# Optimization experiments

Measured on AMD Instinct MI355X. Metric: run time of the kernel, lower is better.

Reference implementation:

```python
import jax, jax.numpy as jnp
import numpy as np

C1 = C2 = COUT = 32
LMAX = 2
N = 8192
FEAT1 = 2 * (1 + 3 + 9) * C1  # 832
WBLK = COUT * C1 * C2


def _enumerate_paths(Lmax):
    paths = []
    for L1 in range(Lmax + 1):
        for L2 in range(Lmax + 1):
            for k in range(min(L1, L2) + 1):
                Lout = L1 + L2 - 2 * k
                if 0 <= Lout <= Lmax:
                    paths.append((L1, L2, Lout, k, False))
            if L1 >= 1 and L2 >= 1:
                for k in range(min(L1 - 1, L2 - 1) + 1):
                    Lout = L1 + L2 - 2 * k - 1
                    if 0 <= Lout <= Lmax:
                        paths.append((L1, L2, Lout, k, True))
    return paths


def _path_eq(L1, L2, k, use_eps):
    # Canonical einsum for one path, fused with the weight mixing 'Zab'
    letters = 'abcdefghijklmnopqrstuvwxyz'
    tl = [c for c in letters if c not in ('a', 'b')]
    i_idx = tl[:L1]
    j_idx = tl[L1:L1 + L2]
    pos = L1 + L2
    for r in range(k):  # pairwise delta contractions on trailing indices
        j_idx[L2 - k + r] = i_idx[L1 - k + r]
    i_free = i_idx[:L1 - k]
    j_free = j_idx[:L2 - k]
    eps_terms = []
    if use_eps:
        ie, je = i_free[-1], j_free[-1]
        i_free, j_free = i_free[:-1], j_free[:-1]
        p = tl[pos]
        eps_terms = [p + ie + je]
        out_idx = i_free + j_free + [p]
    else:
        out_idx = i_free + j_free
    in_terms = ['...a' + ''.join(i_idx), '...b' + ''.join(j_idx)] + eps_terms + ['Zab']
    eq = ','.join(in_terms) + '->...Z' + ''.join(out_idx)
    return eq, len(out_idx)


def _epsilon(dtype):
    e = np.zeros((3, 3, 3), np.float32)
    e[0, 1, 2] = e[1, 2, 0] = e[2, 0, 1] = 1.0
    e[0, 2, 1] = e[2, 1, 0] = e[1, 0, 2] = -1.0
    return jnp.asarray(e, dtype=dtype)


def _split(x, C, Lmax):
    # blocks keyed (s, L): s=0 true tensor, s=1 pseudotensor
    batch = x.shape[:-1]
    out = {}
    idx = 0
    for s in (0, 1):
        for L in range(Lmax + 1):
            d = C * 3 ** L
            blk = x[..., idx:idx + d]
            idx += d
            out[(s, L)] = blk.reshape(*batch, C, *((3,) * L))
    return out


def _forward(x1, x2, weight):
    batch = x1.shape[:-1]
    A = _split(x1, C1, LMAX)
    B = _split(x2, C2, LMAX)
    eps = _epsilon(x1.dtype)
    out = {(s, L): jnp.zeros(batch + (COUT,) + (3,) * L, x1.dtype)
           for s in (0, 1) for L in range(LMAX + 1)}
    w_idx = 0
    for (L1, L2, Lout, k, ue) in _enumerate_paths(LMAX):
        eq, _ = _path_eq(L1, L2, k, ue)
        for s1 in (0, 1):
            for s2 in (0, 1):
                Wp = weight[w_idx:w_idx + WBLK].reshape(COUT, C1, C2)
                w_idx += WBLK
                t1 = A[(s1, L1)]
                t2 = B[(s2, L2)]
                if ue:
                    out_c = jnp.einsum(eq, t1, t2, eps, Wp)
                else:
                    out_c = jnp.einsum(eq, t1, t2, Wp)
                s_out = s1 ^ s2 ^ (1 if ue else 0)
                out[(s_out, Lout)] = out[(s_out, Lout)] + out_c
    parts = [out[(s, L)].reshape(*batch, COUT * 3 ** L)
             for s in (0, 1) for L in range(LMAX + 1)]
    return jnp.concatenate(parts, axis=-1)


def setup_inputs() -> dict:
    key = jax.random.key(0)
    k1, k2, k3 = jax.random.split(key, 3)
    n_paths = len(_enumerate_paths(LMAX))  # 15
    wn = n_paths * 4 * WBLK  # 1966080
    x1 = jax.random.normal(k1, (N, FEAT1), dtype=jnp.float32)
    x2 = jax.random.normal(k2, (N, FEAT1), dtype=jnp.float32)
    weight = jax.random.normal(k3, (wn,), dtype=jnp.float32) * 0.02
    return {"x1": x1, "x2": x2, "weight": weight}


def reference(x1, x2, weight):
    return _forward(x1, x2, weight)
```

## Files before the change

### kernel.cpp

```cpp
#include <hip/hip_runtime.h>

#define DEVINL __device__ __forceinline__

typedef unsigned int  uint32;
typedef unsigned short u16;

typedef short bf16x8  __attribute__((ext_vector_type(8)));
typedef float f32x16  __attribute__((ext_vector_type(16)));
typedef float fx2     __attribute__((ext_vector_type(2)));

union U4H { uint4 u; bf16x8 h; };

constexpr int PL1c[15] = {0,0,0,1,1,1,1,1,1,2,2,2,2,2,2};
constexpr int PL2c[15] = {0,1,2,0,1,1,1,2,2,0,1,1,2,2,2};
constexpr int PLOc[15] = {0,1,2,1,2,0,1,1,2,2,1,2,2,0,1};
constexpr int PTc [15] = {1,1,1,1,1,3,2,3,2,1,3,2,3,9,6};
constexpr int PW3c[3]  = {1,3,9};
constexpr int LOFFc[3] = {0,32,128};

constexpr int GCNT[6] = {6,6,12,12,12,12};
constexpr int GNT [6] = {1,1,3,3,9,9};
__device__ const int g_combo[6][12][3] = {
  {{0,0,0},{0,1,1},{5,0,0},{5,1,1},{13,0,0},{13,1,1},
   {0,0,0},{0,0,0},{0,0,0},{0,0,0},{0,0,0},{0,0,0}},
  {{0,0,1},{0,1,0},{5,0,1},{5,1,0},{13,0,1},{13,1,0},
   {0,0,0},{0,0,0},{0,0,0},{0,0,0},{0,0,0},{0,0,0}},
  {{1,0,0},{1,1,1},{3,0,0},{3,1,1},{7,0,0},{7,1,1},{10,0,0},{10,1,1},
   {6,0,1},{6,1,0},{14,0,1},{14,1,0}},
  {{1,0,1},{1,1,0},{3,0,1},{3,1,0},{7,0,1},{7,1,0},{10,0,1},{10,1,0},
   {6,0,0},{6,1,1},{14,0,0},{14,1,1}},
  {{2,0,0},{2,1,1},{4,0,0},{4,1,1},{9,0,0},{9,1,1},{12,0,0},{12,1,1},
   {8,0,1},{8,1,0},{11,0,1},{11,1,0}},
  {{2,0,1},{2,1,0},{4,0,1},{4,1,0},{9,0,1},{9,1,0},{12,0,1},{12,1,0},
   {8,0,0},{8,1,1},{11,0,0},{11,1,1}},
};

struct Terms { int iA[9]; int jB[9]; int sg[9]; };

DEVINL Terms make_terms(int path, int mo) {
  Terms t{};
  switch (path) {
    case 0:  t.iA[0]=0;  t.jB[0]=0;  t.sg[0]=1; break;
    case 1:  t.iA[0]=0;  t.jB[0]=mo; t.sg[0]=1; break;
    case 2:  t.iA[0]=0;  t.jB[0]=mo; t.sg[0]=1; break;
    case 3:  t.iA[0]=mo; t.jB[0]=0;  t.sg[0]=1; break;
    case 4:  t.iA[0]=mo/3; t.jB[0]=mo%3; t.sg[0]=1; break;
    case 5:  for (int v=0;v<3;++v){t.iA[v]=v; t.jB[v]=v; t.sg[v]=1;} break;
    case 6:  {int p=mo,u1=(p+1)%3,u2=(p+2)%3;
              t.iA[0]=u1; t.jB[0]=u2; t.sg[0]= 1;
              t.iA[1]=u2; t.jB[1]=u1; t.sg[1]=-1;} break;
    case 7:  {int x=mo; for(int u=0;u<3;++u){t.iA[u]=u; t.jB[u]=3*x+u; t.sg[u]=1;}} break;
    case 8:  {int x=mo/3,p=mo%3,u1=(p+1)%3,u2=(p+2)%3;
              t.iA[0]=u1; t.jB[0]=3*x+u2; t.sg[0]= 1;
              t.iA[1]=u2; t.jB[1]=3*x+u1; t.sg[1]=-1;} break;
    case 9:  t.iA[0]=mo; t.jB[0]=0; t.sg[0]=1; break;
    case 10: {int u=mo; for(int v=0;v<3;++v){t.iA[v]=3*u+v; t.jB[v]=v; t.sg[v]=1;}} break;
    case 11: {int u=mo/3,p=mo%3,v1=(p+1)%3,v2=(p+2)%3;
              t.iA[0]=3*u+v1; t.jB[0]=v2; t.sg[0]= 1;
              t.iA[1]=3*u+v2; t.jB[1]=v1; t.sg[1]=-1;} break;
    case 12: {int u=mo/3,x=mo%3; for(int v=0;v<3;++v){t.iA[v]=3*u+v; t.jB[v]=3*x+v; t.sg[v]=1;}} break;
    case 13: for (int w=0;w<9;++w){t.iA[w]=w; t.jB[w]=w; t.sg[w]=1;} break;
    case 14: {int p=mo,u1=(p+1)%3,u2=(p+2)%3;
              for(int v=0;v<3;++v){
                t.iA[2*v]  =3*u1+v; t.jB[2*v]  =3*u2+v; t.sg[2*v]  = 1;
                t.iA[2*v+1]=3*u2+v; t.jB[2*v+1]=3*u1+v; t.sg[2*v+1]=-1;}} break;
  }
  return t;
}

DEVINL u16 f2bf(float f) {
  uint32 u = __float_as_uint(f);
  u += 0x7fffu + ((u >> 16) & 1u);
  return (u16)(u >> 16);
}
DEVINL float bf2f(u16 h) { return __uint_as_float(((uint32)h) << 16); }

DEVINL void unpack8(uint4 r, fx2 out[4]) {
  uint32 c[4] = {r.x, r.y, r.z, r.w};
#pragma unroll
  for (int q = 0; q < 4; ++q) {
    out[q].x = __uint_as_float(c[q] << 16);
    out[q].y = __uint_as_float(c[q] & 0xffff0000u);
  }
}

DEVINL bf16x8 packA(const fx2 p[4]) {
  U4H r;
  r.u.x = __builtin_amdgcn_perm(__float_as_uint(p[0].y), __float_as_uint(p[0].x), 0x07060302u);
  r.u.y = __builtin_amdgcn_perm(__float_as_uint(p[1].y), __float_as_uint(p[1].x), 0x07060302u);
  r.u.z = __builtin_amdgcn_perm(__float_as_uint(p[2].y), __float_as_uint(p[2].x), 0x07060302u);
  r.u.w = __builtin_amdgcn_perm(__float_as_uint(p[3].y), __float_as_uint(p[3].x), 0x07060302u);
  return r.h;
}

DEVINL f32x16 mfma32(bf16x8 a, uint4 w, f32x16 c) {
  U4H x; x.u = w;
  return __builtin_amdgcn_mfma_f32_32x32x16_bf16(a, x.h, c, 0, 0, 0);
}

#define X1STRIDE 834

template<int PATH, int MO>
DEVINL void run_combo(int s1, int s2, int n0,
                      const u16* __restrict__ x2t, const u16* x1l,
                      const uint4* __restrict__ wgl,
                      f32x16& acc, int lane, int wv)
{
  constexpr int L1v = PL1c[PATH];
  constexpr int L2v = PL2c[PATH];
  constexpr int T   = PTc[PATH];
  constexpr int P1v = PW3c[L1v];
  constexpr int NCH = (T + 2) / 3;
  const int bh   = wv & 1;
  const int a0   = (wv >> 1) * 8;
  const int nloc = lane & 31;
  const int oct  = lane >> 5;
  const u16* bb = x2t + (size_t)(n0 + nloc) * 832 + s2 * 416 + LOFFc[L2v]
                + bh * 16 + oct * 8;
  const u16* ab = x1l + nloc * X1STRIDE + s1 * 416 + LOFFc[L1v];
  const uint4* wbase = wgl + ((a0 * 2 + bh) << 6) + lane;
  uint4 wf[8];
#pragma unroll
  for (int ia = 0; ia < 8; ++ia)
    wf[ia] = wbase[ia * 128];
  const Terms tm = make_terms(PATH, MO);
#pragma unroll
  for (int tc = 0; tc < NCH; ++tc) {
    const int tlo = tc * 3;
    const int tn  = (T - tlo < 3) ? (T - tlo) : 3;
    fx2 b2[3][4];
#pragma unroll
    for (int u = 0; u < 3; ++u)
      if (u < tn) {
        uint4 rv = *(const uint4*)(bb + tm.jB[tlo + u] * 32);
        unpack8(rv, b2[u]);
      }
#pragma unroll
    for (int ia = 0; ia < 8; ++ia) {
      fx2 p[4];
#pragma unroll
      for (int u = 0; u < 3; ++u) {
        if (u < tn) {
          float av = bf2f(ab[(a0 + ia) * P1v + tm.iA[tlo + u]]);
          if (tm.sg[tlo + u] < 0) av = -av;
          fx2 a2; a2.x = av; a2.y = av;
          if (u == 0) {
#pragma unroll
            for (int q = 0; q < 4; ++q) p[q] = a2 * b2[0][q];
          } else {
#pragma unroll
            for (int q = 0; q < 4; ++q)
              p[q] = __builtin_elementwise_fma(a2, b2[u][q], p[q]);
          }
        }
      }
      acc = mfma32(packA(p), wf[ia], acc);
    }
  }
}

template<int G, int MOB>
DEVINL void process_chunk(int n0, const u16* __restrict__ x2t, const u16* x1l,
                          const uint4* __restrict__ Wb, float* red,
                          float* __restrict__ out, float* __restrict__ sc,
                          int use_sc, int tid, int lane, int wv)
{
  constexpr int lout  = G >> 1;
  constexpr int s_out = G & 1;
  constexpr int NTF   = GNT[G];
  f32x16 acc;
#pragma unroll
  for (int e = 0; e < 16; ++e) acc[e] = 0.f;

#pragma unroll 1
  for (int ci = 0; ci < GCNT[G]; ++ci) {
    const int path = g_combo[G][ci][0];
    const int s1   = g_combo[G][ci][1];
    const int s2   = g_combo[G][ci][2];
    const int pc   = path * 4 + s1 * 2 + s2;
    const uint4* wgl = Wb + ((size_t)pc << 12);
#define RCASE(P) case P: if constexpr (PLOc[P] == lout) \
      run_combo<P, MOB>(s1, s2, n0, x2t, x1l, wgl, acc, lane, wv); break;
    switch (path) {
      RCASE(0) RCASE(1) RCASE(2) RCASE(3) RCASE(4) RCASE(5) RCASE(6) RCASE(7)
      RCASE(8) RCASE(9) RCASE(10) RCASE(11) RCASE(12) RCASE(13) RCASE(14)
    }
#undef RCASE
    __builtin_amdgcn_sched_barrier(0);
  }
  const int col = lane & 31, oct = lane >> 5;
  constexpr int obase = s_out * 416 + LOFFc[lout];
  __syncthreads();
#pragma unroll
  for (int r = 0; r < 16; ++r) {
    int row = (r & 3) + 8 * (r >> 2) + 4 * oct;
    atomicAdd(&red[(col << 5) + ((row + col) & 31)], acc[r]);
  }
  __syncthreads();
  for (int o = tid; o < 1024; o += 512) {
    int row = o & 31;
    int Z   = o >> 5;
    int idx = (Z << 5) + ((row + Z) & 31);
    float v = red[idx];
    red[idx] = 0.f;
    int colx = obase + Z * NTF + MOB;
    if (use_sc) sc[(size_t)colx * 8192 + n0 + row] = v;
    else        out[(size_t)(n0 + row) * 832 + colx] = v;
  }
}

template<int G>
DEVINL void process_group(int n0, const u16* __restrict__ x2t, const u16* x1l,
                          const uint4* __restrict__ Wb, float* red,
                          float* __restrict__ out, float* __restrict__ sc,
                          int use_sc, int tid, int lane, int wv)
{
  process_chunk<G, 0>(n0, x2t, x1l, Wb, red, out, sc, use_sc, tid, lane, wv);
  if constexpr (GNT[G] >= 3) {
    process_chunk<G, 1>(n0, x2t, x1l, Wb, red, out, sc, use_sc, tid, lane, wv);
    process_chunk<G, 2>(n0, x2t, x1l, Wb, red, out, sc, use_sc, tid, lane, wv);
  }
  if constexpr (GNT[G] == 9) {
    process_chunk<G, 3>(n0, x2t, x1l, Wb, red, out, sc, use_sc, tid, lane, wv);
    process_chunk<G, 4>(n0, x2t, x1l, Wb, red, out, sc, use_sc, tid, lane, wv);
    process_chunk<G, 5>(n0, x2t, x1l, Wb, red, out, sc, use_sc, tid, lane, wv);
    process_chunk<G, 6>(n0, x2t, x1l, Wb, red, out, sc, use_sc, tid, lane, wv);
    process_chunk<G, 7>(n0, x2t, x1l, Wb, red, out, sc, use_sc, tid, lane, wv);
    process_chunk<G, 8>(n0, x2t, x1l, Wb, red, out, sc, use_sc, tid, lane, wv);
  }
}

__global__ __launch_bounds__(512, 2)
void k_main(const float* __restrict__ x1, const u16* __restrict__ x2t,
            const uint4* __restrict__ Wb, float* __restrict__ out,
            float* __restrict__ sc, int use_sc)
{
  __shared__ u16   x1l[32 * X1STRIDE];
  __shared__ float red[1024];
  const int tid  = threadIdx.x;
  const int lane = tid & 63, wv = tid >> 6;
  const int half = blockIdx.x >> 8;
  const int n0   = (blockIdx.x & 255) * 32;

  {
    int rr = tid >> 4, c0 = tid & 15;
    const float* src = x1 + (size_t)(n0 + rr) * 832;
#pragma unroll 4
    for (int jj = 0; jj < 52; ++jj) {
      int colx = c0 + jj * 16;
      x1l[rr * X1STRIDE + colx] = f2bf(src[colx]);
    }
  }
  for (int o = tid; o < 1024; o += 512) red[o] = 0.f;
  __syncthreads();

  if (half == 0) {
    process_group<0>(n0, x2t, x1l, Wb, red, out, sc, use_sc, tid, lane, wv);
    process_group<2>(n0, x2t, x1l, Wb, red, out, sc, use_sc, tid, lane, wv);
    process_group<5>(n0, x2t, x1l, Wb, red, out, sc, use_sc, tid, lane, wv);
  } else {
    process_group<1>(n0, x2t, x1l, Wb, red, out, sc, use_sc, tid, lane, wv);
    process_group<3>(n0, x2t, x1l, Wb, red, out, sc, use_sc, tid, lane, wv);
    process_group<4>(n0, x2t, x1l, Wb, red, out, sc, use_sc, tid, lane, wv);
  }
}

__global__ __launch_bounds__(256)
void k_tr(const float* __restrict__ sc, float* __restrict__ out)
{
  __shared__ float tile[32][65];
  const int tid = threadIdx.x;
  const int cb  = blockIdx.x % 26;
  const int nbk = blockIdx.x / 26;
  if (cb >= 26 || nbk >= 128) return;
  const int c0  = cb * 32;
  const int nb  = nbk * 64;
#pragma unroll
  for (int it = 0; it < 8; ++it) {
    int idx = it * 256 + tid;
    int c = idx >> 6, n = idx & 63;
    tile[c][n] = sc[(size_t)(c0 + c) * 8192 + nb + n];
  }
  __syncthreads();
#pragma unroll
  for (int it = 0; it < 8; ++it) {
    int idx = it * 256 + tid;
    int c = idx & 31, n = idx >> 5;
    out[(size_t)(nb + n) * 832 + c0 + c] = tile[c][n];
  }
}

__global__ void k_convw(const float* __restrict__ w, u16* __restrict__ Wb) {
  int o  = blockIdx.x * 1024 + threadIdx.x;
  int j  = o & 7;
  int l  = (o >> 3) & 63;
  int bh = (o >> 9) & 1;
  int a  = (o >> 10) & 31;
  int pc = o >> 15;
  int Z  = l & 31;
  int b  = bh * 16 + ((l >> 5) & 1) * 8 + j;
  float f = w[((size_t)pc << 15) + (size_t)Z * 1024 + a * 32 + b];
  Wb[o] = f2bf(f);
}

__global__ void k_convx2(const float* __restrict__ x2, u16* __restrict__ x2t) {
  int o = blockIdx.x * 1024 + threadIdx.x;
  int n = o / 832; int r = o - n * 832;
  int s = (r >= 416); int r2 = r - s * 416;
  int L = (r2 >= 32) + (r2 >= 128);
  int off = (L == 0) ? 0 : ((L == 1) ? 32 : 128);
  int c = r2 - off;
  int j = c >> 5, b = c & 31;
  int p3 = (L == 0) ? 1 : ((L == 1) ? 3 : 9);
  float f = x2[(size_t)n * 832 + s * 416 + off + b * p3 + j];
  x2t[o] = f2bf(f);
}

extern "C" void kernel_launch(void* const* d_in, const int* in_sizes, int n_in,
                              void* d_out, int out_size, void* d_ws, size_t ws_size,
                              hipStream_t stream) {
  const float* x1 = (const float*)d_in[0];
  const float* x2 = (const float*)d_in[1];
  const float* w  = (const float*)d_in[2];
  float* out = (float*)d_out;
  u16*   Wb  = (u16*)d_ws;
  u16*   x2t = (u16*)((char*)d_ws + (4u << 20));
  float* sc  = (float*)((char*)d_ws + (20u << 20));
  const size_t sc_need = (20u << 20) + (size_t)832 * 8192 * 4;
  const int use_sc = (ws_size >= sc_need) ? 1 : 0;
  (void)in_sizes; (void)n_in; (void)out_size;

  k_convw <<<1920, 1024, 0, stream>>>(w, Wb);
  k_convx2<<<6656, 1024, 0, stream>>>(x2, x2t);
  k_main  <<<512, 512, 0, stream>>>(x1, x2t, (const uint4*)Wb, out, sc, use_sc);
  if (use_sc) k_tr<<<26 * 128, 256, 0, stream>>>(sc, out);
}
```

Measured before the change: 756.5 us.

## Process three output components per pass and transpose x1 tile in LDS

Each chunk now accumulates three output tensor components at once in separate MFMA accumulators, so weight fragments loaded per combo are reused three times instead of being reloaded per component. The x1 tile in shared memory is stored channel-contiguous per tensor component, so each lane fetches its eight channels with two 64-bit LDS loads instead of scalar 16-bit loads. The cost is three times the accumulator registers, which is why launch bounds drop to one block per CU at 512 threads.

```diff
diff --git a/kernel.cpp b/kernel.cpp
--- a/kernel.cpp
+++ b/kernel.cpp
@@ -73,7 +73,6 @@
   u += 0x7fffu + ((u >> 16) & 1u);
   return (u16)(u >> 16);
 }
-DEVINL float bf2f(u16 h) { return __uint_as_float(((uint32)h) << 16); }
 
 DEVINL void unpack8(uint4 r, fx2 out[4]) {
   uint32 c[4] = {r.x, r.y, r.z, r.w};
@@ -98,18 +97,17 @@
   return __builtin_amdgcn_mfma_f32_32x32x16_bf16(a, x.h, c, 0, 0, 0);
 }
 
-#define X1STRIDE 834
-
-template<int PATH, int MO>
+#define X1STRIDE 836
+
+template<int PATH, int NTC, int MOB>
 DEVINL void run_combo(int s1, int s2, int n0,
                       const u16* __restrict__ x2t, const u16* x1l,
                       const uint4* __restrict__ wgl,
-                      f32x16& acc, int lane, int wv)
+                      f32x16* acc, int lane, int wv)
 {
   constexpr int L1v = PL1c[PATH];
   constexpr int L2v = PL2c[PATH];
   constexpr int T   = PTc[PATH];
-  constexpr int P1v = PW3c[L1v];
   constexpr int NCH = (T + 2) / 3;
   const int bh   = wv & 1;
   const int a0   = (wv >> 1) * 8;
@@ -117,49 +115,59 @@
   const int oct  = lane >> 5;
   const u16* bb = x2t + (size_t)(n0 + nloc) * 832 + s2 * 416 + LOFFc[L2v]
                 + bh * 16 + oct * 8;
-  const u16* ab = x1l + nloc * X1STRIDE + s1 * 416 + LOFFc[L1v];
+  const u16* ab = x1l + nloc * X1STRIDE + s1 * 416 + LOFFc[L1v] + a0;
   const uint4* wbase = wgl + ((a0 * 2 + bh) << 6) + lane;
   uint4 wf[8];
 #pragma unroll
   for (int ia = 0; ia < 8; ++ia)
     wf[ia] = wbase[ia * 128];
-  const Terms tm = make_terms(PATH, MO);
-#pragma unroll
-  for (int tc = 0; tc < NCH; ++tc) {
-    const int tlo = tc * 3;
-    const int tn  = (T - tlo < 3) ? (T - tlo) : 3;
-    fx2 b2[3][4];
-#pragma unroll
-    for (int u = 0; u < 3; ++u)
-      if (u < tn) {
-        uint4 rv = *(const uint4*)(bb + tm.jB[tlo + u] * 32);
-        unpack8(rv, b2[u]);
-      }
-#pragma unroll
-    for (int ia = 0; ia < 8; ++ia) {
-      fx2 p[4];
-#pragma unroll
-      for (int u = 0; u < 3; ++u) {
+#pragma unroll
+  for (int m = 0; m < NTC; ++m) {
+    const Terms tm = make_terms(PATH, MOB + m);
+#pragma unroll
+    for (int tc = 0; tc < NCH; ++tc) {
+      const int tlo = tc * 3;
+      const int tn  = (T - tlo < 3) ? (T - tlo) : 3;
+      fx2 b2[3][4];
+      uint2 alo[3], ahi[3];
+#pragma unroll
+      for (int u = 0; u < 3; ++u)
         if (u < tn) {
-          float av = bf2f(ab[(a0 + ia) * P1v + tm.iA[tlo + u]]);
-          if (tm.sg[tlo + u] < 0) av = -av;
-          fx2 a2; a2.x = av; a2.y = av;
-          if (u == 0) {
-#pragma unroll
-            for (int q = 0; q < 4; ++q) p[q] = a2 * b2[0][q];
-          } else {
-#pragma unroll
-            for (int q = 0; q < 4; ++q)
-              p[q] = __builtin_elementwise_fma(a2, b2[u][q], p[q]);
+          uint4 rv = *(const uint4*)(bb + tm.jB[tlo + u] * 32);
+          unpack8(rv, b2[u]);
+          const u16* ap = ab + tm.iA[tlo + u] * 32;
+          alo[u] = *(const uint2*)(ap);
+          ahi[u] = *(const uint2*)(ap + 4);
+        }
+#pragma unroll
+      for (int ia = 0; ia < 8; ++ia) {
+        fx2 p[4];
+#pragma unroll
+        for (int u = 0; u < 3; ++u) {
+          if (u < tn) {
+            uint32 wrd = (ia < 2) ? alo[u].x : (ia < 4) ? alo[u].y
+                       : (ia < 6) ? ahi[u].x : ahi[u].y;
+            float av = (ia & 1) ? __uint_as_float(wrd & 0xffff0000u)
+                                : __uint_as_float(wrd << 16);
+            if (tm.sg[tlo + u] < 0) av = -av;
+            fx2 a2; a2.x = av; a2.y = av;
+            if (u == 0) {
+#pragma unroll
+              for (int q = 0; q < 4; ++q) p[q] = a2 * b2[0][q];
+            } else {
+#pragma unroll
+              for (int q = 0; q < 4; ++q)
+                p[q] = __builtin_elementwise_fma(a2, b2[u][q], p[q]);
+            }
           }
         }
+        acc[m] = mfma32(packA(p), wf[ia], acc[m]);
       }
-      acc = mfma32(packA(p), wf[ia], acc);
-    }
-  }
-}
-
-template<int G, int MOB>
+    }
+  }
+}
+
+template<int G, int MOB, int NTC>
 DEVINL void process_chunk(int n0, const u16* __restrict__ x2t, const u16* x1l,
                           const uint4* __restrict__ Wb, float* red,
                           float* __restrict__ out, float* __restrict__ sc,
@@ -168,9 +176,11 @@
   constexpr int lout  = G >> 1;
   constexpr int s_out = G & 1;
   constexpr int NTF   = GNT[G];
-  f32x16 acc;
-#pragma unroll
-  for (int e = 0; e < 16; ++e) acc[e] = 0.f;
+  f32x16 acc[NTC];
+#pragma unroll
+  for (int t = 0; t < NTC; ++t)
+#pragma unroll
+    for (int e = 0; e < 16; ++e) acc[t][e] = 0.f;
 
 #pragma unroll 1
   for (int ci = 0; ci < GCNT[G]; ++ci) {
@@ -180,7 +190,7 @@
     const int pc   = path * 4 + s1 * 2 + s2;
     const uint4* wgl = Wb + ((size_t)pc << 12);
 #define RCASE(P) case P: if constexpr (PLOc[P] == lout) \
-      run_combo<P, MOB>(s1, s2, n0, x2t, x1l, wgl, acc, lane, wv); break;
+      run_combo<P, NTC, MOB>(s1, s2, n0, x2t, x1l, wgl, acc, lane, wv); break;
     switch (path) {
       RCASE(0) RCASE(1) RCASE(2) RCASE(3) RCASE(4) RCASE(5) RCASE(6) RCASE(7)
       RCASE(8) RCASE(9) RCASE(10) RCASE(11) RCASE(12) RCASE(13) RCASE(14)
@@ -190,47 +200,29 @@
   }
   const int col = lane & 31, oct = lane >> 5;
   constexpr int obase = s_out * 416 + LOFFc[lout];
-  __syncthreads();
-#pragma unroll
-  for (int r = 0; r < 16; ++r) {
-    int row = (r & 3) + 8 * (r >> 2) + 4 * oct;
-    atomicAdd(&red[(col << 5) + ((row + col) & 31)], acc[r]);
-  }
-  __syncthreads();
-  for (int o = tid; o < 1024; o += 512) {
-    int row = o & 31;
-    int Z   = o >> 5;
-    int idx = (Z << 5) + ((row + Z) & 31);
-    float v = red[idx];
-    red[idx] = 0.f;
-    int colx = obase + Z * NTF + MOB;
-    if (use_sc) sc[(size_t)colx * 8192 + n0 + row] = v;
-    else        out[(size_t)(n0 + row) * 832 + colx] = v;
-  }
-}
-
-template<int G>
-DEVINL void process_group(int n0, const u16* __restrict__ x2t, const u16* x1l,
-                          const uint4* __restrict__ Wb, float* red,
-                          float* __restrict__ out, float* __restrict__ sc,
-                          int use_sc, int tid, int lane, int wv)
-{
-  process_chunk<G, 0>(n0, x2t, x1l, Wb, red, out, sc, use_sc, tid, lane, wv);
-  if constexpr (GNT[G] >= 3) {
-    process_chunk<G, 1>(n0, x2t, x1l, Wb, red, out, sc, use_sc, tid, lane, wv);
-    process_chunk<G, 2>(n0, x2t, x1l, Wb, red, out, sc, use_sc, tid, lane, wv);
-  }
-  if constexpr (GNT[G] == 9) {
-    process_chunk<G, 3>(n0, x2t, x1l, Wb, red, out, sc, use_sc, tid, lane, wv);
-    process_chunk<G, 4>(n0, x2t, x1l, Wb, red, out, sc, use_sc, tid, lane, wv);
-    process_chunk<G, 5>(n0, x2t, x1l, Wb, red, out, sc, use_sc, tid, lane, wv);
-    process_chunk<G, 6>(n0, x2t, x1l, Wb, red, out, sc, use_sc, tid, lane, wv);
-    process_chunk<G, 7>(n0, x2t, x1l, Wb, red, out, sc, use_sc, tid, lane, wv);
-    process_chunk<G, 8>(n0, x2t, x1l, Wb, red, out, sc, use_sc, tid, lane, wv);
-  }
-}
-
-__global__ __launch_bounds__(512, 2)
+#pragma unroll 1
+  for (int t = 0; t < NTC; ++t) {
+    __syncthreads();
+#pragma unroll
+    for (int r = 0; r < 16; ++r) {
+      int row = (r & 3) + 8 * (r >> 2) + 4 * oct;
+      atomicAdd(&red[(col << 5) + ((row + col) & 31)], acc[t][r]);
+    }
+    __syncthreads();
+    for (int o = tid; o < 1024; o += 512) {
+      int row = o & 31;
+      int Z   = o >> 5;
+      int idx = (Z << 5) + ((row + Z) & 31);
+      float v = red[idx];
+      red[idx] = 0.f;
+      int colx = obase + Z * NTF + MOB + t;
+      if (use_sc) sc[(size_t)colx * 8192 + n0 + row] = v;
+      else        out[(size_t)(n0 + row) * 832 + colx] = v;
+    }
+  }
+}
+
+__global__ __launch_bounds__(512, 1)
 void k_main(const float* __restrict__ x1, const u16* __restrict__ x2t,
             const uint4* __restrict__ Wb, float* __restrict__ out,
             float* __restrict__ sc, int use_sc)
@@ -247,21 +239,32 @@
     const float* src = x1 + (size_t)(n0 + rr) * 832;
 #pragma unroll 4
     for (int jj = 0; jj < 52; ++jj) {
-      int colx = c0 + jj * 16;
-      x1l[rr * X1STRIDE + colx] = f2bf(src[colx]);
+      int d  = c0 + jj * 16;
+      int s  = (d >= 416);
+      int d2 = d - s * 416;
+      int L  = (d2 >= 32) + (d2 >= 128);
+      int off = (L == 0) ? 0 : ((L == 1) ? 32 : 128);
+      int dl = d2 - off;
+      int i  = dl >> 5, a = dl & 31;
+      int p3 = (L == 0) ? 1 : ((L == 1) ? 3 : 9);
+      x1l[rr * X1STRIDE + d] = f2bf(src[s * 416 + off + a * p3 + i]);
     }
   }
   for (int o = tid; o < 1024; o += 512) red[o] = 0.f;
   __syncthreads();
 
   if (half == 0) {
-    process_group<0>(n0, x2t, x1l, Wb, red, out, sc, use_sc, tid, lane, wv);
-    process_group<2>(n0, x2t, x1l, Wb, red, out, sc, use_sc, tid, lane, wv);
-    process_group<5>(n0, x2t, x1l, Wb, red, out, sc, use_sc, tid, lane, wv);
+    process_chunk<0, 0, 1>(n0, x2t, x1l, Wb, red, out, sc, use_sc, tid, lane, wv);
+    process_chunk<2, 0, 3>(n0, x2t, x1l, Wb, red, out, sc, use_sc, tid, lane, wv);
+    process_chunk<5, 0, 3>(n0, x2t, x1l, Wb, red, out, sc, use_sc, tid, lane, wv);
+    process_chunk<5, 3, 3>(n0, x2t, x1l, Wb, red, out, sc, use_sc, tid, lane, wv);
+    process_chunk<5, 6, 3>(n0, x2t, x1l, Wb, red, out, sc, use_sc, tid, lane, wv);
   } else {
-    process_group<1>(n0, x2t, x1l, Wb, red, out, sc, use_sc, tid, lane, wv);
-    process_group<3>(n0, x2t, x1l, Wb, red, out, sc, use_sc, tid, lane, wv);
-    process_group<4>(n0, x2t, x1l, Wb, red, out, sc, use_sc, tid, lane, wv);
+    process_chunk<1, 0, 1>(n0, x2t, x1l, Wb, red, out, sc, use_sc, tid, lane, wv);
+    process_chunk<3, 0, 3>(n0, x2t, x1l, Wb, red, out, sc, use_sc, tid, lane, wv);
+    process_chunk<4, 0, 3>(n0, x2t, x1l, Wb, red, out, sc, use_sc, tid, lane, wv);
+    process_chunk<4, 3, 3>(n0, x2t, x1l, Wb, red, out, sc, use_sc, tid, lane, wv);
+    process_chunk<4, 6, 3>(n0, x2t, x1l, Wb, red, out, sc, use_sc, tid, lane, wv);
   }
 }
 
```

New measurement: 904.7 us. +19.6%, slower.
